# Kernel tuning notes

Hardware: AMD Instinct MI355X
Metric: run time of the kernel (lower is better)

## Reference

```python
import jax, jax.numpy as jnp
import numpy as np

N_MET, N_RXN, D, C, H, E = 20000, 40000, 256, 64, 4, 250000
P = 0.2  # MC dropout prob (always active)


def setup_inputs() -> dict:
    key = jax.random.key(0)
    ks = jax.random.split(key, 40)
    g = lambda i, shape: jax.random.normal(ks[i], shape, jnp.float32) * 0.05
    inp = {
        'x_met': jax.random.normal(ks[0], (N_MET, D), jnp.float32),
        'x_rxn': jax.random.normal(ks[1], (N_RXN, D), jnp.float32),
        'sub_src': jax.random.randint(ks[2], (E,), 0, N_MET),
        'sub_dst': jax.random.randint(ks[3], (E,), 0, N_RXN),
        'prod_src': jax.random.randint(ks[4], (E,), 0, N_RXN),
        'prod_dst': jax.random.randint(ks[5], (E,), 0, N_MET),
        'shr_src': jax.random.randint(ks[6], (E,), 0, N_RXN),
        'shr_dst': jax.random.randint(ks[7], (E,), 0, N_RXN),
    }
    i = 8
    for name in ['sub', 'prod', 'shr']:
        inp['Wl_' + name] = g(i, (D, H * C)); inp['bl_' + name] = g(i + 1, (H * C,))
        inp['Wr_' + name] = g(i + 2, (D, H * C)); inp['br_' + name] = g(i + 3, (H * C,))
        inp['att_' + name] = g(i + 4, (H, C)); inp['b_' + name] = g(i + 5, (C,))
        i += 6
    inp['W_proj_rxn'] = g(26, (D, C)); inp['b_proj_rxn'] = g(27, (C,))
    inp['W_proj_met'] = g(28, (D, C)); inp['b_proj_met'] = g(29, (C,))
    inp['ln_rxn_g'] = jnp.ones((C,), jnp.float32); inp['ln_rxn_b'] = jnp.zeros((C,), jnp.float32)
    inp['ln_met_g'] = jnp.ones((C,), jnp.float32); inp['ln_met_b'] = jnp.zeros((C,), jnp.float32)
    return inp


def gatv2(xs, xd, src, dst, Wl, bl, Wr, br, att, bias, n_dst):
    # GATv2Conv (concat=False): mean over heads, eval-mode attention (no attn dropout).
    Hh, Cc = att.shape
    xl = (xs @ Wl + bl).reshape(xs.shape[0], Hh, Cc)  # source transform
    xr = (xd @ Wr + br).reshape(xd.shape[0], Hh, Cc)  # destination transform
    s = jax.nn.leaky_relu(xl[src] + xr[dst], 0.2)     # [E,H,C]
    e = jnp.einsum('ehc,hc->eh', s, att)              # [E,H] per-edge scores
    m = jax.ops.segment_max(e, dst, num_segments=n_dst)
    m = jnp.where(jnp.isfinite(m), m, 0.0)            # nodes with no in-edges
    ex = jnp.exp(e - m[dst])
    den = jax.ops.segment_sum(ex, dst, num_segments=n_dst)
    alpha = ex / (den[dst] + 1e-16)                   # segment softmax (PyG eps)
    out = jax.ops.segment_sum(alpha[:, :, None] * xl[src], dst, num_segments=n_dst)
    return out.mean(axis=1) + bias                    # [n_dst, C]


def layernorm(x, g, b):
    mu = x.mean(-1, keepdims=True)
    var = x.var(-1, keepdims=True)
    return (x - mu) * jax.lax.rsqrt(var + 1e-5) * g + b


def mc_dropout(x, key):
    mask = jax.random.bernoulli(key, 1.0 - P, x.shape)
    return jnp.where(mask, x / (1.0 - P), 0.0)


def reference(x_met, x_rxn, sub_src, sub_dst, prod_src, prod_dst, shr_src, shr_dst,
              Wl_sub, bl_sub, Wr_sub, br_sub, att_sub, b_sub,
              Wl_prod, bl_prod, Wr_prod, br_prod, att_prod, b_prod,
              Wl_shr, bl_shr, Wr_shr, br_shr, att_shr, b_shr,
              W_proj_rxn, b_proj_rxn, W_proj_met, b_proj_met,
              ln_rxn_g, ln_rxn_b, ln_met_g, ln_met_b):
    # shared_metabolite relation: add_self_loops=True
    sl = jnp.arange(N_RXN, dtype=shr_src.dtype)
    shr_src_f = jnp.concatenate([shr_src, sl])
    shr_dst_f = jnp.concatenate([shr_dst, sl])

    out_sub = gatv2(x_met, x_rxn, sub_src, sub_dst, Wl_sub, bl_sub, Wr_sub, br_sub, att_sub, b_sub, N_RXN)
    out_shr = gatv2(x_rxn, x_rxn, shr_src_f, shr_dst_f, Wl_shr, bl_shr, Wr_shr, br_shr, att_shr, b_shr, N_RXN)
    out_prod = gatv2(x_rxn, x_met, prod_src, prod_dst, Wl_prod, bl_prod, Wr_prod, br_prod, att_prod, b_prod, N_MET)

    rxn = 0.5 * (out_sub + out_shr)  # HeteroConv aggr='mean' over 2 relations
    met = out_prod                   # single relation -> mean is identity

    rxn = layernorm(jax.nn.elu(rxn) + (x_rxn @ W_proj_rxn + b_proj_rxn), ln_rxn_g, ln_rxn_b)
    met = layernorm(jax.nn.elu(met) + (x_met @ W_proj_met + b_proj_met), ln_met_g, ln_met_b)

    k1, k2 = jax.random.split(jax.random.key(1))
    return mc_dropout(rxn, k1), mc_dropout(met, k2)
```

## Files before the change

kernel.cpp:

```cpp
#include <hip/hip_runtime.h>
#include <hip/hip_bf16.h>
#include <stdint.h>

#define NMET 20000
#define NRXN 40000
#define DDIM 256
#define CDIM 64

typedef __attribute__((ext_vector_type(8))) short bf16x8;
typedef __attribute__((ext_vector_type(4))) float f32x4;

typedef __attribute__((address_space(1))) const void gvoid_t;
typedef __attribute__((address_space(3))) void lvoid_t;

__host__ __device__ inline void tf2x32(unsigned k0, unsigned k1,
                                       unsigned x0, unsigned x1,
                                       unsigned &o0, unsigned &o1) {
  unsigned ks2 = k0 ^ k1 ^ 0x1BD11BDAu;
#define TFR(r) { x0 += x1; x1 = (x1 << r) | (x1 >> (32 - r)); x1 ^= x0; }
  x0 += k0; x1 += k1;
  TFR(13) TFR(15) TFR(26) TFR(6)
  x0 += k1; x1 += ks2 + 1u;
  TFR(17) TFR(29) TFR(16) TFR(24)
  x0 += ks2; x1 += k0 + 2u;
  TFR(13) TFR(15) TFR(26) TFR(6)
  x0 += k0; x1 += k1 + 3u;
  TFR(17) TFR(29) TFR(16) TFR(24)
  x0 += k1; x1 += ks2 + 4u;
  TFR(13) TFR(15) TFR(26) TFR(6)
  x0 += ks2; x1 += k0 + 5u;
#undef TFR
  o0 = x0; o1 = x1;
}

__device__ inline unsigned short f2bbits(float f) {
  __hip_bfloat16 h = __float2bfloat16(f);
  return *reinterpret_cast<unsigned short*>(&h);
}
__device__ inline float b2f(unsigned short u) {
  unsigned v = (unsigned)u << 16;
  return __uint_as_float(v);
}

#define CVT_A_BLK 2500
#define CVT_B_BLK 5000
__global__ __launch_bounds__(256) void prep_all(
    const float* __restrict__ x_met, __hip_bfloat16* __restrict__ xmb,
    const float* __restrict__ x_rxn, __hip_bfloat16* __restrict__ xrb,
    const float* w0, const float* w1, const float* w2, const float* w3,
    const float* w4, const float* w5, const float* w6, const float* w7,
    __hip_bfloat16* o0, __hip_bfloat16* o1, __hip_bfloat16* o2, __hip_bfloat16* o3,
    __hip_bfloat16* o4, __hip_bfloat16* o5, __hip_bfloat16* o6, __hip_bfloat16* o7) {
  __shared__ float ts[32][33];
  int bid = blockIdx.x;
  if (bid < CVT_A_BLK + CVT_B_BLK) {
    const float* in; __hip_bfloat16* out; int n;
    if (bid < CVT_A_BLK) { in = x_met; out = xmb; n = NMET * DDIM; }
    else { in = x_rxn; out = xrb; n = NRXN * DDIM; bid -= CVT_A_BLK; }
    int i = (bid * 256 + threadIdx.x) * 8;
    if (i >= n) return;
    float4 va = *reinterpret_cast<const float4*>(in + i);
    float4 vb = *reinterpret_cast<const float4*>(in + i + 4);
    bf16x8 o;
    o[0] = (short)f2bbits(va.x); o[1] = (short)f2bbits(va.y);
    o[2] = (short)f2bbits(va.z); o[3] = (short)f2bbits(va.w);
    o[4] = (short)f2bbits(vb.x); o[5] = (short)f2bbits(vb.y);
    o[6] = (short)f2bbits(vb.z); o[7] = (short)f2bbits(vb.w);
    *reinterpret_cast<bf16x8*>(out + i) = o;
    return;
  }
  int t = bid - (CVT_A_BLK + CVT_B_BLK);
  int z = t >> 6, tt = t & 63;
  const float* w; __hip_bfloat16* o; int Ncols;
  switch (z) {
    case 0: w = w0; o = o0; Ncols = 256; break;
    case 1: w = w1; o = o1; Ncols = 256; break;
    case 2: w = w2; o = o2; Ncols = 256; break;
    case 3: w = w3; o = o3; Ncols = 256; break;
    case 4: w = w4; o = o4; Ncols = 256; break;
    case 5: w = w5; o = o5; Ncols = 256; break;
    case 6: w = w6; o = o6; Ncols = 64; break;
    default: w = w7; o = o7; Ncols = 64; break;
  }
  int ntile = Ncols / 32;
  if (tt >= ntile * 8) return;
  int tn = tt % ntile, tk = tt / ntile;
  int tx = threadIdx.x & 31, ty = threadIdx.x >> 5;
#pragma unroll
  for (int r = ty; r < 32; r += 8)
    ts[r][tx] = w[(size_t)(tk * 32 + r) * Ncols + tn * 32 + tx];
  __syncthreads();
#pragma unroll
  for (int r = ty; r < 32; r += 8)
    o[(size_t)(tn * 32 + r) * 256 + tk * 32 + tx] = __float2bfloat16(ts[tx][r]);
}

struct TDesc {
  const __hip_bfloat16* X;
  const __hip_bfloat16* W;
  const float* bias;
  __hip_bfloat16* Yb;
  float* Yf;
  int M, N, nt, blocks;
};
struct TD8 { TDesc g[8]; };

__global__ __launch_bounds__(256) void gemm_tiled8(TD8 gd, int ng) {
  __shared__ __align__(16) char As[2][16384];
  __shared__ __align__(16) char Bs[2][16384];
  int bid = blockIdx.x;
  int di = 0;
  while (di < ng && bid >= gd.g[di].blocks) { bid -= gd.g[di].blocks; ++di; }
  if (di >= ng) return;
  TDesc g = gd.g[di];
  int mrow = bid / g.nt, ntile = bid - mrow * g.nt;
  int m0 = mrow * 128, n0 = ntile * 128;
  int tid = threadIdx.x, wave = tid >> 6, lane = tid & 63;
  int lr = lane & 15, lk = lane >> 4;
  int wm = wave >> 1, wn = wave & 1;
  int brows = g.N - n0; if (brows > 128) brows = 128;
  int bch = brows >> 3;
  int lrow = lane >> 3;
  int gsw = ((lane & 7) ^ lrow) * 8;

  auto stage = [&](int buf, int kt) {
    for (int c = wave; c < 16; c += 4) {
      int row = m0 + c * 8 + lrow;
      if (row > g.M - 1) row = g.M - 1;
      const void* src = g.X + (size_t)row * DDIM + kt * 64 + gsw;
      __builtin_amdgcn_global_load_lds((gvoid_t*)src, (lvoid_t*)(As[buf] + c * 1024), 16, 0, 0);
    }
    for (int c = wave; c < bch; c += 4) {
      int row = n0 + c * 8 + lrow;
      const void* src = g.W + (size_t)row * DDIM + kt * 64 + gsw;
      __builtin_amdgcn_global_load_lds((gvoid_t*)src, (lvoid_t*)(Bs[buf] + c * 1024), 16, 0, 0);
    }
  };

  f32x4 acc[4][4] = {};
  stage(0, 0);
  __syncthreads();
#pragma unroll
  for (int kt = 0; kt < 4; ++kt) {
    int cur = kt & 1;
    if (kt < 3) stage(cur ^ 1, kt + 1);
#pragma unroll
    for (int kk = 0; kk < 2; ++kk) {
      bf16x8 a[4], b[4];
#pragma unroll
      for (int m = 0; m < 4; ++m) {
        int row = wm * 64 + m * 16 + lr;
        int grp = (kk * 4 + lk) ^ (lr & 7);
        a[m] = *reinterpret_cast<const bf16x8*>(As[cur] + row * 128 + grp * 16);
      }
#pragma unroll
      for (int n = 0; n < 4; ++n) {
        int row = wn * 64 + n * 16 + lr;
        int grp = (kk * 4 + lk) ^ (lr & 7);
        b[n] = *reinterpret_cast<const bf16x8*>(Bs[cur] + row * 128 + grp * 16);
      }
#pragma unroll
      for (int m = 0; m < 4; ++m)
#pragma unroll
        for (int n = 0; n < 4; ++n)
          acc[m][n] = __builtin_amdgcn_mfma_f32_16x16x32_bf16(a[m], b[n], acc[m][n], 0, 0, 0);
    }
    __syncthreads();
  }
  bool isb = (g.Yb != nullptr);
#pragma unroll
  for (int m = 0; m < 4; ++m) {
#pragma unroll
    for (int rr = 0; rr < 4; ++rr) {
      int row = m0 + wm * 64 + m * 16 + lk * 4 + rr;
      if (row >= g.M) continue;
#pragma unroll
      for (int n = 0; n < 4; ++n) {
        int cg = n0 + wn * 64 + n * 16 + lr;
        if (cg >= g.N) continue;
        float v = acc[m][n][rr] + g.bias[cg];
        if (isb) g.Yb[(size_t)row * g.N + cg] = __float2bfloat16(v);
        else     g.Yf[(size_t)row * g.N + cg] = v;
      }
    }
  }
}

__global__ __launch_bounds__(256) void hist3(
    const int* __restrict__ d0, const int* __restrict__ d1, const int* __restrict__ d2,
    int E, int* __restrict__ c0, int* __restrict__ c1, int* __restrict__ c2) {
  int i = blockIdx.x * 256 + threadIdx.x;
  if (i >= E) return;
  int rel = blockIdx.y;
  if (rel == 0) atomicAdd(&c0[d0[i]], 1);
  else if (rel == 1) atomicAdd(&c1[d1[i]], 1);
  else atomicAdd(&c2[d2[i]], 1);
}

__global__ __launch_bounds__(256) void alloc3(
    const int* __restrict__ c0, const int* __restrict__ c1, const int* __restrict__ c2,
    int* __restrict__ o0, int* __restrict__ o1, int* __restrict__ o2,
    int* __restrict__ u0, int* __restrict__ u1, int* __restrict__ u2,
    int* __restrict__ cursors, int n0, int n1, int n2) {
  int rel = blockIdx.y;
  int i = blockIdx.x * 256 + threadIdx.x;
  const int* c = (rel == 0) ? c0 : (rel == 1) ? c1 : c2;
  int* o = (rel == 0) ? o0 : (rel == 1) ? o1 : o2;
  int* u = (rel == 0) ? u0 : (rel == 1) ? u1 : u2;
  int n = (rel == 0) ? n0 : (rel == 1) ? n1 : n2;
  if (i >= n) return;
  int cc = c[i];
  int pos = atomicAdd(&cursors[rel], cc);
  o[i] = pos; u[i] = pos;
}

__global__ __launch_bounds__(256) void scatter3(
    const int* __restrict__ s0, const int* __restrict__ d0,
    const int* __restrict__ s1, const int* __restrict__ d1,
    const int* __restrict__ s2, const int* __restrict__ d2,
    int E, int* __restrict__ u0, int* __restrict__ u1, int* __restrict__ u2,
    int* __restrict__ e0, int* __restrict__ e1, int* __restrict__ e2) {
  int i = blockIdx.x * 256 + threadIdx.x;
  if (i >= E) return;
  int rel = blockIdx.y;
  if (rel == 0)      { int pos = atomicAdd(&u0[d0[i]], 1); e0[pos] = s0[i]; }
  else if (rel == 1) { int pos = atomicAdd(&u1[d1[i]], 1); e1[pos] = s1[i]; }
  else               { int pos = atomicAdd(&u2[d2[i]], 1); e2[pos] = s2[i]; }
}

struct GatRel {
  const __hip_bfloat16* xl;
  const __hip_bfloat16* xr;
  const int* off; const int* cnt; const int* srce;
  const float* att; float* acc;
  int n; int self_loop;
};

__global__ __launch_bounds__(256) void gat3(GatRel r0, GatRel r1, GatRel r2) {
  int gidx = blockIdx.x * 4 + (threadIdx.x >> 6);
  int lane = threadIdx.x & 63;
  GatRel r; int d;
  if (gidx < r0.n) { r = r0; d = gidx; }
  else if (gidx < r0.n + r1.n) { r = r1; d = gidx - r0.n; }
  else if (gidx < r0.n + r1.n + r2.n) { r = r2; d = gidx - r0.n - r1.n; }
  else return;

  ushort4 ur = *reinterpret_cast<const ushort4*>(r.xr + (size_t)d * DDIM + 4 * lane);
  float c0 = b2f(ur.x), c1 = b2f(ur.y), c2 = b2f(ur.z), c3 = b2f(ur.w);
  float4 at = *reinterpret_cast<const float4*>(r.att + 4 * lane);

  float den = 0.f;
  float a0 = 0.f, a1 = 0.f, a2 = 0.f, a3 = 0.f;

#define EBODY(ux) {                                                             \
    float x0 = b2f(ux.x), x1 = b2f(ux.y), x2 = b2f(ux.z), x3 = b2f(ux.w);       \
    float t0 = x0 + c0; t0 = fmaxf(t0, 0.2f * t0);                              \
    float t1 = x1 + c1; t1 = fmaxf(t1, 0.2f * t1);                              \
    float t2 = x2 + c2; t2 = fmaxf(t2, 0.2f * t2);                              \
    float t3 = x3 + c3; t3 = fmaxf(t3, 0.2f * t3);                              \
    float pp = t0 * at.x + t1 * at.y + t2 * at.z + t3 * at.w;                   \
    pp += __shfl_xor(pp, 1); pp += __shfl_xor(pp, 2);                           \
    pp += __shfl_xor(pp, 4); pp += __shfl_xor(pp, 8);                           \
    float ex = __expf(pp);                                                      \
    den += ex;                                                                  \
    a0 = fmaf(ex, x0, a0); a1 = fmaf(ex, x1, a1);                               \
    a2 = fmaf(ex, x2, a2); a3 = fmaf(ex, x3, a3);                               \
  }
#define ELOAD(s_) *reinterpret_cast<const ushort4*>(r.xl + (size_t)(s_) * DDIM + 4 * lane)

  if (r.self_loop) { ushort4 ux = ELOAD(d); EBODY(ux) }
  int cnt = r.cnt[d];
  int beg = r.off[d];
  for (int jb = 0; jb < cnt; jb += 64) {
    int jj = jb + lane; if (jj > cnt - 1) jj = cnt - 1;
    int srcv = r.srce[beg + jj];
    int lim = cnt - jb; if (lim > 64) lim = 64;
    int u = 0;
    for (; u + 4 <= lim; u += 4) {
      int s0 = __shfl(srcv, u), s1 = __shfl(srcv, u + 1);
      int s2 = __shfl(srcv, u + 2), s3 = __shfl(srcv, u + 3);
      ushort4 ux0 = ELOAD(s0); ushort4 ux1 = ELOAD(s1);
      ushort4 ux2 = ELOAD(s2); ushort4 ux3 = ELOAD(s3);
      EBODY(ux0) EBODY(ux1) EBODY(ux2) EBODY(ux3)
    }
    for (; u < lim; ++u) {
      int s = __shfl(srcv, u);
      ushort4 ux = ELOAD(s); EBODY(ux)
    }
  }
#undef EBODY
#undef ELOAD

  float inv = (den > 0.f) ? 1.0f / den : 0.f;
  float p0 = a0 * inv, p1 = a1 * inv, p2 = a2 * inv, p3 = a3 * inv;
  p0 += __shfl_xor(p0, 16); p0 += __shfl_xor(p0, 32);
  p1 += __shfl_xor(p1, 16); p1 += __shfl_xor(p1, 32);
  p2 += __shfl_xor(p2, 16); p2 += __shfl_xor(p2, 32);
  p3 += __shfl_xor(p3, 16); p3 += __shfl_xor(p3, 32);
  int srcl = lane >> 2;
  float v0 = __shfl(p0, srcl);
  float v1 = __shfl(p1, srcl);
  float v2 = __shfl(p2, srcl);
  float v3 = __shfl(p3, srcl);
  float val = (lane & 2) ? ((lane & 1) ? v3 : v2) : ((lane & 1) ? v1 : v0);
  r.acc[(size_t)d * 64 + lane] = 0.25f * val;
}

struct FDesc {
  const float* accA; const float* accB;
  float* out;
  const float* bA; const float* bB; float scale;
  const float* g; const float* be;
  int n; unsigned key0, key1;
};

__global__ __launch_bounds__(256) void finalize2(FDesc f0, FDesc f1) {
  int gidx = blockIdx.x * 4 + (threadIdx.x >> 6);
  int lane = threadIdx.x & 63;
  FDesc f; int d;
  if (gidx < f0.n) { f = f0; d = gidx; }
  else if (gidx < f0.n + f1.n) { f = f1; d = gidx - f0.n; }
  else return;
  unsigned idx = (unsigned)d * 64u + (unsigned)lane;
  float bias = f.bA[lane] + (f.bB ? f.bB[lane] : 0.f);
  float agg = f.accA[idx] + (f.accB ? f.accB[idx] : 0.f);
  float pre = f.scale * (agg + bias);
  pre = (pre > 0.f) ? pre : expm1f(pre);
  pre += f.out[idx];
  float mu = pre;
#pragma unroll
  for (int off = 32; off; off >>= 1) mu += __shfl_xor(mu, off);
  mu *= (1.0f / 64.0f);
  float dv = pre - mu;
  float var = dv * dv;
#pragma unroll
  for (int off = 32; off; off >>= 1) var += __shfl_xor(var, off);
  var *= (1.0f / 64.0f);
  float y = dv * rsqrtf(var + 1e-5f) * f.g[lane] + f.be[lane];
  unsigned o0, o1;
  tf2x32(f.key0, f.key1, 0u, idx, o0, o1);
  unsigned bits = o0 ^ o1;
  float u = __uint_as_float((bits >> 9) | 0x3f800000u) - 1.0f;
  y = (u < 0.8f) ? y / 0.8f : 0.0f;
  f.out[idx] = y;
}

extern "C" void kernel_launch(void* const* d_in, const int* in_sizes, int n_in,
                              void* d_out, int out_size, void* d_ws, size_t ws_size,
                              hipStream_t stream) {
  const float* x_met = (const float*)d_in[0];
  const float* x_rxn = (const float*)d_in[1];
  const int* sub_src = (const int*)d_in[2];
  const int* sub_dst = (const int*)d_in[3];
  const int* prod_src = (const int*)d_in[4];
  const int* prod_dst = (const int*)d_in[5];
  const int* shr_src = (const int*)d_in[6];
  const int* shr_dst = (const int*)d_in[7];
  const float* Wl_sub = (const float*)d_in[8];
  const float* bl_sub = (const float*)d_in[9];
  const float* Wr_sub = (const float*)d_in[10];
  const float* br_sub = (const float*)d_in[11];
  const float* att_sub = (const float*)d_in[12];
  const float* b_sub = (const float*)d_in[13];
  const float* Wl_prod = (const float*)d_in[14];
  const float* bl_prod = (const float*)d_in[15];
  const float* Wr_prod = (const float*)d_in[16];
  const float* br_prod = (const float*)d_in[17];
  const float* att_prod = (const float*)d_in[18];
  const float* b_prod = (const float*)d_in[19];
  const float* Wl_shr = (const float*)d_in[20];
  const float* bl_shr = (const float*)d_in[21];
  const float* Wr_shr = (const float*)d_in[22];
  const float* br_shr = (const float*)d_in[23];
  const float* att_shr = (const float*)d_in[24];
  const float* b_shr = (const float*)d_in[25];
  const float* W_proj_rxn = (const float*)d_in[26];
  const float* b_proj_rxn = (const float*)d_in[27];
  const float* W_proj_met = (const float*)d_in[28];
  const float* b_proj_met = (const float*)d_in[29];
  const float* ln_rxn_g = (const float*)d_in[30];
  const float* ln_rxn_b = (const float*)d_in[31];
  const float* ln_met_g = (const float*)d_in[32];
  const float* ln_met_b = (const float*)d_in[33];

  const int E = in_sizes[2];

  char* p = (char*)d_ws;
  auto take = [&](size_t b) { char* q = p; p += (b + 255) & ~(size_t)255; return q; };
  __hip_bfloat16* xmb = (__hip_bfloat16*)take((size_t)NMET * DDIM * 2);
  __hip_bfloat16* xrb = (__hip_bfloat16*)take((size_t)NRXN * DDIM * 2);
  __hip_bfloat16* wt[8];
  for (int i = 0; i < 6; ++i) wt[i] = (__hip_bfloat16*)take(256 * 256 * 2);
  for (int i = 6; i < 8; ++i) wt[i] = (__hip_bfloat16*)take(64 * 256 * 2);
  float* acc_sub = (float*)take((size_t)NRXN * CDIM * 4);
  float* acc_shr = (float*)take((size_t)NRXN * CDIM * 4);
  float* acc_met = (float*)take((size_t)NMET * CDIM * 4);
  int* cnt_sub = (int*)take((size_t)NRXN * 4 + (size_t)NRXN * 4 + (size_t)NMET * 4 + 16);
  int* cnt_shr = cnt_sub + NRXN;
  int* cnt_prod = cnt_shr + NRXN;
  int* cursors = cnt_prod + NMET;
  int* off_sub = (int*)take((size_t)NRXN * 4);
  int* off_shr = (int*)take((size_t)NRXN * 4);
  int* off_prod = (int*)take((size_t)NMET * 4);
  int* cur_sub = (int*)take((size_t)NRXN * 4);
  int* cur_shr = (int*)take((size_t)NRXN * 4);
  int* cur_prod = (int*)take((size_t)NMET * 4);
  int* srce_sub = (int*)take((size_t)E * 4);
  int* srce_shr = (int*)take((size_t)E * 4);
  int* srce_prod = (int*)take((size_t)E * 4);

  size_t met_b = (size_t)NMET * DDIM * 2, rxn_b = (size_t)NRXN * DDIM * 2;
  size_t used = (size_t)(p - (char*)d_ws);
  bool big = (ws_size >= used + 3 * met_b + 3 * rxn_b + 4096);

  __hip_bfloat16 *xl_sub, *xr_sub, *xl_shr, *xr_shr, *xl_prod, *xr_prod;
  if (big) {
    xl_sub = (__hip_bfloat16*)take(met_b);
    xr_sub = (__hip_bfloat16*)take(rxn_b);
    xl_shr = (__hip_bfloat16*)take(rxn_b);
    xr_shr = (__hip_bfloat16*)take(rxn_b);
    xl_prod = (__hip_bfloat16*)take(rxn_b);
    xr_prod = (__hip_bfloat16*)take(met_b);
  } else {
    __hip_bfloat16* xa = (__hip_bfloat16*)take(rxn_b);
    __hip_bfloat16* xb = (__hip_bfloat16*)take(rxn_b);
    xl_sub = xl_shr = xl_prod = xa;
    xr_sub = xr_shr = xr_prod = xb;
  }

  float* out_rxn = (float*)d_out;
  float* out_met = out_rxn + (size_t)NRXN * CDIM;

  unsigned k1_0, k1_1, k2_0, k2_1;
  tf2x32(0u, 1u, 0u, 0u, k1_0, k1_1);
  tf2x32(0u, 1u, 0u, 1u, k2_0, k2_1);

  dim3 blk(256);

  hipMemsetAsync(cnt_sub, 0, ((size_t)(NRXN + NRXN + NMET) + 4) * 4, stream);
  hist3<<<dim3((E + 255) / 256, 3), blk, 0, stream>>>(
      sub_dst, shr_dst, prod_dst, E, cnt_sub, cnt_shr, cnt_prod);
  alloc3<<<dim3((NRXN + 255) / 256, 3), blk, 0, stream>>>(
      cnt_sub, cnt_shr, cnt_prod, off_sub, off_shr, off_prod,
      cur_sub, cur_shr, cur_prod, cursors, NRXN, NRXN, NMET);
  prep_all<<<CVT_A_BLK + CVT_B_BLK + 512, blk, 0, stream>>>(
      x_met, xmb, x_rxn, xrb,
      Wl_sub, Wr_sub, Wl_shr, Wr_shr, Wl_prod, Wr_prod, W_proj_rxn, W_proj_met,
      wt[0], wt[1], wt[2], wt[3], wt[4], wt[5], wt[6], wt[7]);
  scatter3<<<dim3((E + 255) / 256, 3), blk, 0, stream>>>(
      sub_src, sub_dst, shr_src, shr_dst, prod_src, prod_dst, E,
      cur_sub, cur_shr, cur_prod, srce_sub, srce_shr, srce_prod);

  auto mk = [](const __hip_bfloat16* X, const __hip_bfloat16* W, const float* bias,
               __hip_bfloat16* Yb, float* Yf, int M, int N) {
    TDesc g; g.X = X; g.W = W; g.bias = bias; g.Yb = Yb; g.Yf = Yf;
    g.M = M; g.N = N; g.nt = (N + 127) / 128;
    g.blocks = ((M + 127) / 128) * g.nt;
    return g;
  };
  auto mkrel = [](const __hip_bfloat16* xl, const __hip_bfloat16* xr,
                  const int* off, const int* cnt, const int* srce,
                  const float* att, float* acc, int n, int sl) {
    GatRel r; r.xl = xl; r.xr = xr; r.off = off; r.cnt = cnt; r.srce = srce;
    r.att = att; r.acc = acc; r.n = n; r.self_loop = sl;
    return r;
  };
  GatRel rz{}; rz.n = 0;

  TDesc dsub_r  = mk(xrb, wt[1], br_sub,     xr_sub,  nullptr, NRXN, DDIM);
  TDesc dshr_l  = mk(xrb, wt[2], bl_shr,     xl_shr,  nullptr, NRXN, DDIM);
  TDesc dshr_r  = mk(xrb, wt[3], br_shr,     xr_shr,  nullptr, NRXN, DDIM);
  TDesc dprod_l = mk(xrb, wt[4], bl_prod,    xl_prod, nullptr, NRXN, DDIM);
  TDesc dproj_r = mk(xrb, wt[6], b_proj_rxn, nullptr, out_rxn, NRXN, CDIM);
  TDesc dsub_l  = mk(xmb, wt[0], bl_sub,     xl_sub,  nullptr, NMET, DDIM);
  TDesc dprod_m = mk(xmb, wt[5], br_prod,    xr_prod, nullptr, NMET, DDIM);
  TDesc dproj_m = mk(xmb, wt[7], b_proj_met, nullptr, out_met, NMET, CDIM);

  GatRel rsub = mkrel(xl_sub, xr_sub, off_sub, cnt_sub, srce_sub, att_sub, acc_sub, NRXN, 0);
  GatRel rshr = mkrel(xl_shr, xr_shr, off_shr, cnt_shr, srce_shr, att_shr, acc_shr, NRXN, 1);
  GatRel rprod = mkrel(xl_prod, xr_prod, off_prod, cnt_prod, srce_prod, att_prod, acc_met, NMET, 0);

  if (big) {
    TD8 gd = {{dsub_r, dshr_l, dshr_r, dprod_l, dproj_r, dsub_l, dprod_m, dproj_m}};
    int tot = 0;
    for (int i = 0; i < 8; ++i) tot += gd.g[i].blocks;
    gemm_tiled8<<<tot, blk, 0, stream>>>(gd, 8);
    gat3<<<(NRXN + NRXN + NMET + 3) / 4, blk, 0, stream>>>(rsub, rshr, rprod);
  } else {
    TD8 gd1 = {{dproj_r, dproj_m, dsub_l, dsub_r}};
    int t1 = gd1.g[0].blocks + gd1.g[1].blocks + gd1.g[2].blocks + gd1.g[3].blocks;
    gemm_tiled8<<<t1, blk, 0, stream>>>(gd1, 4);
    gat3<<<(NRXN + 3) / 4, blk, 0, stream>>>(rsub, rz, rz);
    TD8 gd2 = {{dshr_l, dshr_r}};
    int t2 = gd2.g[0].blocks + gd2.g[1].blocks;
    gemm_tiled8<<<t2, blk, 0, stream>>>(gd2, 2);
    gat3<<<(NRXN + 3) / 4, blk, 0, stream>>>(rshr, rz, rz);
    TD8 gd3 = {{dprod_l, dprod_m}};
    int t3 = gd3.g[0].blocks + gd3.g[1].blocks;
    gemm_tiled8<<<t3, blk, 0, stream>>>(gd3, 2);
    gat3<<<(NMET + 3) / 4, blk, 0, stream>>>(rprod, rz, rz);
  }

  FDesc f0, f1;
  f0.accA = acc_sub; f0.accB = acc_shr; f0.out = out_rxn;
  f0.bA = b_sub; f0.bB = b_shr; f0.scale = 0.5f;
  f0.g = ln_rxn_g; f0.be = ln_rxn_b; f0.n = NRXN; f0.key0 = k1_0; f0.key1 = k1_1;
  f1.accA = acc_met; f1.accB = nullptr; f1.out = out_met;
  f1.bA = b_prod; f1.bB = nullptr; f1.scale = 1.0f;
  f1.g = ln_met_g; f1.be = ln_met_b; f1.n = NMET; f1.key0 = k2_0; f1.key1 = k2_1;
  finalize2<<<(NRXN + NMET + 3) / 4, blk, 0, stream>>>(f0, f1);
}
```

Before: 370.1 us.

## Replace tiled multi-GEMM with panel GEMM keeping full X rows in LDS

In the big path, each block now loads a 64-row panel of the input (full K=256) into LDS once and computes every weight's output tiles for it, reading B fragments straight from global/L2. Each X row is read once instead of once per output tile and weight. The old tiled kernel also loses its double buffering, so loads and MFMA no longer overlap there, but that kernel now runs only on the non-big path. Reading B from global per wave may become latency-bound.

```diff
diff --git a/kernel.cpp b/kernel.cpp
--- a/kernel.cpp
+++ b/kernel.cpp
@@ -95,6 +95,81 @@
     o[(size_t)(tn * 32 + r) * 256 + tk * 32 + tx] = __float2bfloat16(ts[tx][r]);
 }
 
+struct PanelDesc {
+  const __hip_bfloat16* X; int M; int mblocks; int nw; int ntiles;
+  const __hip_bfloat16* W[5]; const float* bias[5];
+  __hip_bfloat16* Yb[5]; float* Yf[5]; int N[5];
+};
+
+__global__ __launch_bounds__(256) void gemm_panel(PanelDesc p0, PanelDesc p1) {
+  __shared__ __align__(16) char As[32768];
+  int bid = blockIdx.x;
+  PanelDesc pd = (bid < p0.mblocks) ? p0 : p1;
+  if (bid >= p0.mblocks) bid -= p0.mblocks;
+  int m0 = bid * 64;
+  int tid = threadIdx.x, wave = tid >> 6, lane = tid & 63;
+  int lr = lane & 15, lk = lane >> 4;
+
+#pragma unroll
+  for (int i = 0; i < 8; ++i) {
+    int c = wave * 8 + i;
+    int r = 2 * c + (lane >> 5);
+    int grow = m0 + r; if (grow > pd.M - 1) grow = pd.M - 1;
+    int gcol = ((lane & 31) ^ (r & 7)) * 8;
+    const void* src = pd.X + (size_t)grow * DDIM + gcol;
+    __builtin_amdgcn_global_load_lds((gvoid_t*)src, (lvoid_t*)(As + c * 1024), 16, 0, 0);
+  }
+  __syncthreads();
+
+  for (int tt = wave; tt < pd.ntiles; tt += 4) {
+    int wi = 0, nt = tt;
+    while (nt >= (pd.N[wi] >> 6)) { nt -= (pd.N[wi] >> 6); ++wi; }
+    int n0 = nt * 64;
+    const __hip_bfloat16* Wp = pd.W[wi];
+    int Nw = pd.N[wi];
+
+    f32x4 acc[4][4] = {};
+#pragma unroll
+    for (int ks = 0; ks < 8; ++ks) {
+      bf16x8 a[4], b[4];
+#pragma unroll
+      for (int m = 0; m < 4; ++m) {
+        int row = m * 16 + lr;
+        int gp = (ks * 4 + lk) ^ (row & 7);
+        a[m] = *reinterpret_cast<const bf16x8*>(As + row * 512 + gp * 16);
+      }
+#pragma unroll
+      for (int j = 0; j < 4; ++j)
+        b[j] = *reinterpret_cast<const bf16x8*>(
+            Wp + (size_t)(n0 + j * 16 + lr) * DDIM + ks * 32 + lk * 8);
+#pragma unroll
+      for (int m = 0; m < 4; ++m)
+#pragma unroll
+        for (int j = 0; j < 4; ++j)
+          acc[m][j] = __builtin_amdgcn_mfma_f32_16x16x32_bf16(a[m], b[j], acc[m][j], 0, 0, 0);
+    }
+    const float* bias = pd.bias[wi];
+    __hip_bfloat16* Yb = pd.Yb[wi];
+    float* Yf = pd.Yf[wi];
+    bool isb = (Yb != nullptr);
+#pragma unroll
+    for (int m = 0; m < 4; ++m) {
+#pragma unroll
+      for (int rr = 0; rr < 4; ++rr) {
+        int row = m0 + m * 16 + lk * 4 + rr;
+        if (row >= pd.M) continue;
+#pragma unroll
+        for (int j = 0; j < 4; ++j) {
+          int col = n0 + j * 16 + lr;
+          float v = acc[m][j][rr] + bias[col];
+          if (isb) Yb[(size_t)row * Nw + col] = __float2bfloat16(v);
+          else     Yf[(size_t)row * Nw + col] = v;
+        }
+      }
+    }
+  }
+}
+
 struct TDesc {
   const __hip_bfloat16* X;
   const __hip_bfloat16* W;
@@ -106,8 +181,8 @@
 struct TD8 { TDesc g[8]; };
 
 __global__ __launch_bounds__(256) void gemm_tiled8(TD8 gd, int ng) {
-  __shared__ __align__(16) char As[2][16384];
-  __shared__ __align__(16) char Bs[2][16384];
+  __shared__ __align__(16) char As[16384];
+  __shared__ __align__(16) char Bs[16384];
   int bid = blockIdx.x;
   int di = 0;
   while (di < ng && bid >= gd.g[di].blocks) { bid -= gd.g[di].blocks; ++di; }
@@ -123,27 +198,20 @@
   int lrow = lane >> 3;
   int gsw = ((lane & 7) ^ lrow) * 8;
 
-  auto stage = [&](int buf, int kt) {
+  f32x4 acc[4][4] = {};
+  for (int kt = 0; kt < 4; ++kt) {
     for (int c = wave; c < 16; c += 4) {
       int row = m0 + c * 8 + lrow;
       if (row > g.M - 1) row = g.M - 1;
       const void* src = g.X + (size_t)row * DDIM + kt * 64 + gsw;
-      __builtin_amdgcn_global_load_lds((gvoid_t*)src, (lvoid_t*)(As[buf] + c * 1024), 16, 0, 0);
+      __builtin_amdgcn_global_load_lds((gvoid_t*)src, (lvoid_t*)(As + c * 1024), 16, 0, 0);
     }
     for (int c = wave; c < bch; c += 4) {
       int row = n0 + c * 8 + lrow;
       const void* src = g.W + (size_t)row * DDIM + kt * 64 + gsw;
-      __builtin_amdgcn_global_load_lds((gvoid_t*)src, (lvoid_t*)(Bs[buf] + c * 1024), 16, 0, 0);
-    }
-  };
-
-  f32x4 acc[4][4] = {};
-  stage(0, 0);
-  __syncthreads();
-#pragma unroll
-  for (int kt = 0; kt < 4; ++kt) {
-    int cur = kt & 1;
-    if (kt < 3) stage(cur ^ 1, kt + 1);
+      __builtin_amdgcn_global_load_lds((gvoid_t*)src, (lvoid_t*)(Bs + c * 1024), 16, 0, 0);
+    }
+    __syncthreads();
 #pragma unroll
     for (int kk = 0; kk < 2; ++kk) {
       bf16x8 a[4], b[4];
@@ -151,13 +219,13 @@
       for (int m = 0; m < 4; ++m) {
         int row = wm * 64 + m * 16 + lr;
         int grp = (kk * 4 + lk) ^ (lr & 7);
-        a[m] = *reinterpret_cast<const bf16x8*>(As[cur] + row * 128 + grp * 16);
+        a[m] = *reinterpret_cast<const bf16x8*>(As + row * 128 + grp * 16);
       }
 #pragma unroll
       for (int n = 0; n < 4; ++n) {
         int row = wn * 64 + n * 16 + lr;
         int grp = (kk * 4 + lk) ^ (lr & 7);
-        b[n] = *reinterpret_cast<const bf16x8*>(Bs[cur] + row * 128 + grp * 16);
+        b[n] = *reinterpret_cast<const bf16x8*>(Bs + row * 128 + grp * 16);
       }
 #pragma unroll
       for (int m = 0; m < 4; ++m)
@@ -451,13 +519,6 @@
       sub_src, sub_dst, shr_src, shr_dst, prod_src, prod_dst, E,
       cur_sub, cur_shr, cur_prod, srce_sub, srce_shr, srce_prod);
 
-  auto mk = [](const __hip_bfloat16* X, const __hip_bfloat16* W, const float* bias,
-               __hip_bfloat16* Yb, float* Yf, int M, int N) {
-    TDesc g; g.X = X; g.W = W; g.bias = bias; g.Yb = Yb; g.Yf = Yf;
-    g.M = M; g.N = N; g.nt = (N + 127) / 128;
-    g.blocks = ((M + 127) / 128) * g.nt;
-    return g;
-  };
   auto mkrel = [](const __hip_bfloat16* xl, const __hip_bfloat16* xr,
                   const int* off, const int* cnt, const int* srce,
                   const float* att, float* acc, int n, int sl) {
@@ -467,26 +528,42 @@
   };
   GatRel rz{}; rz.n = 0;
 
-  TDesc dsub_r  = mk(xrb, wt[1], br_sub,     xr_sub,  nullptr, NRXN, DDIM);
-  TDesc dshr_l  = mk(xrb, wt[2], bl_shr,     xl_shr,  nullptr, NRXN, DDIM);
-  TDesc dshr_r  = mk(xrb, wt[3], br_shr,     xr_shr,  nullptr, NRXN, DDIM);
-  TDesc dprod_l = mk(xrb, wt[4], bl_prod,    xl_prod, nullptr, NRXN, DDIM);
-  TDesc dproj_r = mk(xrb, wt[6], b_proj_rxn, nullptr, out_rxn, NRXN, CDIM);
-  TDesc dsub_l  = mk(xmb, wt[0], bl_sub,     xl_sub,  nullptr, NMET, DDIM);
-  TDesc dprod_m = mk(xmb, wt[5], br_prod,    xr_prod, nullptr, NMET, DDIM);
-  TDesc dproj_m = mk(xmb, wt[7], b_proj_met, nullptr, out_met, NMET, CDIM);
-
   GatRel rsub = mkrel(xl_sub, xr_sub, off_sub, cnt_sub, srce_sub, att_sub, acc_sub, NRXN, 0);
   GatRel rshr = mkrel(xl_shr, xr_shr, off_shr, cnt_shr, srce_shr, att_shr, acc_shr, NRXN, 1);
   GatRel rprod = mkrel(xl_prod, xr_prod, off_prod, cnt_prod, srce_prod, att_prod, acc_met, NMET, 0);
 
   if (big) {
-    TD8 gd = {{dsub_r, dshr_l, dshr_r, dprod_l, dproj_r, dsub_l, dprod_m, dproj_m}};
-    int tot = 0;
-    for (int i = 0; i < 8; ++i) tot += gd.g[i].blocks;
-    gemm_tiled8<<<tot, blk, 0, stream>>>(gd, 8);
+    PanelDesc pr{}, pm{};
+    pr.X = xrb; pr.M = NRXN; pr.mblocks = (NRXN + 63) / 64;
+    pr.nw = 5; pr.ntiles = 4 + 4 + 4 + 4 + 1;
+    pr.W[0] = wt[1]; pr.bias[0] = br_sub;     pr.Yb[0] = xr_sub;  pr.Yf[0] = nullptr; pr.N[0] = DDIM;
+    pr.W[1] = wt[2]; pr.bias[1] = bl_shr;     pr.Yb[1] = xl_shr;  pr.Yf[1] = nullptr; pr.N[1] = DDIM;
+    pr.W[2] = wt[3]; pr.bias[2] = br_shr;     pr.Yb[2] = xr_shr;  pr.Yf[2] = nullptr; pr.N[2] = DDIM;
+    pr.W[3] = wt[4]; pr.bias[3] = bl_prod;    pr.Yb[3] = xl_prod; pr.Yf[3] = nullptr; pr.N[3] = DDIM;
+    pr.W[4] = wt[6]; pr.bias[4] = b_proj_rxn; pr.Yb[4] = nullptr; pr.Yf[4] = out_rxn; pr.N[4] = CDIM;
+    pm.X = xmb; pm.M = NMET; pm.mblocks = (NMET + 63) / 64;
+    pm.nw = 3; pm.ntiles = 4 + 4 + 1;
+    pm.W[0] = wt[0]; pm.bias[0] = bl_sub;     pm.Yb[0] = xl_sub;  pm.Yf[0] = nullptr; pm.N[0] = DDIM;
+    pm.W[1] = wt[5]; pm.bias[1] = br_prod;    pm.Yb[1] = xr_prod; pm.Yf[1] = nullptr; pm.N[1] = DDIM;
+    pm.W[2] = wt[7]; pm.bias[2] = b_proj_met; pm.Yb[2] = nullptr; pm.Yf[2] = out_met; pm.N[2] = CDIM;
+    gemm_panel<<<pr.mblocks + pm.mblocks, blk, 0, stream>>>(pr, pm);
     gat3<<<(NRXN + NRXN + NMET + 3) / 4, blk, 0, stream>>>(rsub, rshr, rprod);
   } else {
+    auto mk = [](const __hip_bfloat16* X, const __hip_bfloat16* W, const float* bias,
+                 __hip_bfloat16* Yb, float* Yf, int M, int N) {
+      TDesc g; g.X = X; g.W = W; g.bias = bias; g.Yb = Yb; g.Yf = Yf;
+      g.M = M; g.N = N; g.nt = (N + 127) / 128;
+      g.blocks = ((M + 127) / 128) * g.nt;
+      return g;
+    };
+    TDesc dsub_r  = mk(xrb, wt[1], br_sub,     xr_sub,  nullptr, NRXN, DDIM);
+    TDesc dshr_l  = mk(xrb, wt[2], bl_shr,     xl_shr,  nullptr, NRXN, DDIM);
+    TDesc dshr_r  = mk(xrb, wt[3], br_shr,     xr_shr,  nullptr, NRXN, DDIM);
+    TDesc dprod_l = mk(xrb, wt[4], bl_prod,    xl_prod, nullptr, NRXN, DDIM);
+    TDesc dproj_r = mk(xrb, wt[6], b_proj_rxn, nullptr, out_rxn, NRXN, CDIM);
+    TDesc dsub_l  = mk(xmb, wt[0], bl_sub,     xl_sub,  nullptr, NMET, DDIM);
+    TDesc dprod_m = mk(xmb, wt[5], br_prod,    xr_prod, nullptr, NMET, DDIM);
+    TDesc dproj_m = mk(xmb, wt[7], b_proj_met, nullptr, out_met, NMET, CDIM);
     TD8 gd1 = {{dproj_r, dproj_m, dsub_l, dsub_r}};
     int t1 = gd1.g[0].blocks + gd1.g[1].blocks + gd1.g[2].blocks + gd1.g[3].blocks;
     gemm_tiled8<<<t1, blk, 0, stream>>>(gd1, 4);
```

Result: slower. 395.5 us (+6.9%).
